# Kernel optimization log

Hardware: AMD Instinct MI355X
Metric: run time of the kernel (lower is better)

The kernel has to match this reference:

```python
import jax, jax.numpy as jnp
import numpy as np

N = 128
INSTANCES = 64
EMBED_DIM = 256
HIDDEN = 1024
BATCH = 2048


def _kaiming(key, dims):
    # matches custom_kaiming: randn * sqrt(2 / dims[-2])
    return jax.random.normal(key, dims, dtype=jnp.float32) * np.sqrt(2.0 / float(dims[-2])).astype(np.float32)


def setup_inputs() -> dict:
    key = jax.random.key(0)
    k_a, k_el, k_er, k_lin, k_un = jax.random.split(key, 5)
    a = jax.random.randint(k_a, (BATCH, 2), 0, N, dtype=jnp.int64 if jax.config.jax_enable_x64 else jnp.int32)
    return {
        "a": a,
        "embedding_left": _kaiming(k_el, (INSTANCES, N, EMBED_DIM)),
        "embedding_right": _kaiming(k_er, (INSTANCES, N, EMBED_DIM)),
        "linear": _kaiming(k_lin, (INSTANCES, EMBED_DIM, HIDDEN)),
        "unembedding": _kaiming(k_un, (INSTANCES, HIDDEN, N)),
    }


def reference(a, embedding_left, embedding_right, linear, unembedding):
    # one-hot @ embedding == direct gather along the vocab axis (same math, O(1) per lookup)
    a1, a2 = a[:, 0], a[:, 1]
    # [instances, batch, embed] -> [batch, instances, embed]
    x1 = jnp.transpose(jnp.take(embedding_left, a1, axis=1), (1, 0, 2))
    x2 = jnp.transpose(jnp.take(embedding_right, a2, axis=1), (1, 0, 2))
    hidden = jnp.einsum('bie,ieh->bih', x1 + x2, linear)
    out = jnp.einsum('bih,ihn->bin', jax.nn.gelu(hidden, approximate=False), unembedding)
    return out
```

## Files before the change

### kernel.cpp

```cpp
#include <hip/hip_runtime.h>
#include <hip/hip_bf16.h>

typedef __bf16 bf16;
typedef __bf16 bf16x8 __attribute__((ext_vector_type(8)));
typedef float  f32x4  __attribute__((ext_vector_type(4)));

#define MFMA16(A,B,C) __builtin_amdgcn_mfma_f32_16x16x32_bf16((A),(B),(C),0,0,0)

constexpr int NI    = 64;
constexpr int NN    = 128;
constexpr int E     = 256;
constexpr int HID   = 1024;
constexpr int BATCH = 2048;
constexpr int BM    = 128;
constexpr int BH    = 64;
constexpr int W1P   = E  + 8;
constexpr int W2P   = BH + 8;
constexpr int HP    = BH + 8;

__global__ __launch_bounds__(256) void transpose_cvt(
    const float* __restrict__ in, bf16* __restrict__ out, int R, int C)
{
    __shared__ bf16 t[64][74];
    const int inst = blockIdx.z;
    const int r0 = blockIdx.y * 64, c0 = blockIdx.x * 64;
    const float* ip = in + ((size_t)inst * R + r0) * C + c0;
    #pragma unroll
    for (int it = 0; it < 4; ++it) {
        int idx = it * 256 + threadIdx.x;
        int r = idx >> 4, c4 = idx & 15;
        f32x4 v = *(const f32x4*)(ip + (size_t)r * C + c4 * 4);
        #pragma unroll
        for (int k = 0; k < 4; ++k) t[r][c4 * 4 + k] = (bf16)v[k];
    }
    __syncthreads();
    bf16* op = out + ((size_t)inst * C + c0) * R + r0;
    #pragma unroll
    for (int it = 0; it < 2; ++it) {
        int idx = it * 256 + threadIdx.x;
        int c = idx >> 3, r8 = idx & 7;
        bf16x8 tmp;
        #pragma unroll
        for (int k = 0; k < 8; ++k) tmp[k] = t[r8 * 8 + k][c];
        *(bf16x8*)(op + (size_t)c * R + r8 * 8) = tmp;
    }
}

__device__ __forceinline__ float fast_gelu(float x) {
    float p = 1.5957691216f * __builtin_fmaf(0.044715f * x * x, x, x);
    return x * __builtin_amdgcn_rcpf(1.0f + __expf(-p));
}

template <bool PRET>
__global__ __launch_bounds__(256, 2) void mlp3_fused(
    const int*   __restrict__ a,
    const float* __restrict__ embL,
    const float* __restrict__ embR,
    const void*  __restrict__ W1v,
    const void*  __restrict__ W2v,
    float* __restrict__ out)
{
    __shared__ __align__(16) bf16 sW1[BH][W1P];
    __shared__ __align__(16) bf16 sW2[NN][W2P];
    __shared__ __align__(16) bf16 sH [BM][HP];
    static_assert(sizeof(bf16) * (BH * W1P + NN * W2P + BM * HP) <= 80 * 1024, "2 blocks/CU");

    const int blk   = blockIdx.x;
    const int xcd   = blk & 7;
    const int j     = blk >> 3;
    const int inst  = xcd + 8 * (j >> 4);
    const int btile = j & 15;

    const int tid  = threadIdx.x;
    const int wave = tid >> 6;
    const int lane = tid & 63;
    const int m = lane & 15;
    const int q = lane >> 4;

    bf16x8 aF[2][8];
    #pragma unroll
    for (int rt = 0; rt < 2; ++rt) {
        const int r  = btile * BM + wave * 32 + rt * 16 + m;
        const int i1 = a[2 * r + 0];
        const int i2 = a[2 * r + 1];
        const float* pl = embL + ((size_t)inst * NN + i1) * E;
        const float* pr = embR + ((size_t)inst * NN + i2) * E;
        #pragma unroll
        for (int ks = 0; ks < 8; ++ks) {
            const int e0 = ks * 32 + q * 8;
            f32x4 l0 = *(const f32x4*)(pl + e0);
            f32x4 l1 = *(const f32x4*)(pl + e0 + 4);
            f32x4 r0 = *(const f32x4*)(pr + e0);
            f32x4 r1 = *(const f32x4*)(pr + e0 + 4);
            bf16x8 s;
            #pragma unroll
            for (int k = 0; k < 4; ++k) {
                s[k]     = (bf16)(l0[k] + r0[k]);
                s[k + 4] = (bf16)(l1[k] + r1[k]);
            }
            aF[rt][ks] = s;
        }
    }

    f32x4 O[2][8];
    #pragma unroll
    for (int rt = 0; rt < 2; ++rt)
        #pragma unroll
        for (int ct = 0; ct < 8; ++ct)
            O[rt][ct] = (f32x4){0.f, 0.f, 0.f, 0.f};

    #pragma unroll 1
    for (int c = 0; c < HID / BH; ++c) {
        __syncthreads();
        if (PRET) {
            const bf16* W1 = (const bf16*)W1v;
            const bf16* W2 = (const bf16*)W2v;
            #pragma unroll
            for (int it = 0; it < 8; ++it) {
                const int idx = it * 256 + tid;
                const int hl = idx >> 5, e16 = idx & 31;
                *(bf16x8*)&sW1[hl][e16 * 8] =
                    *(const bf16x8*)(W1 + ((size_t)inst * HID + c * BH + hl) * E + e16 * 8);
            }
            #pragma unroll
            for (int it = 0; it < 4; ++it) {
                const int idx = it * 256 + tid;
                const int n = idx >> 3, h8 = idx & 7;
                *(bf16x8*)&sW2[n][h8 * 8] =
                    *(const bf16x8*)(W2 + ((size_t)inst * NN + n) * HID + c * BH + h8 * 8);
            }
        } else {
            const float* W1 = (const float*)W1v;
            const float* W2 = (const float*)W2v;
            #pragma unroll
            for (int it = 0; it < 8; ++it) {
                const int idx = it * 256 + tid;
                const int e = idx >> 3, h8 = idx & 7;
                f32x4 v0 = *(const f32x4*)(W1 + ((size_t)inst * E + e) * HID + c * BH + h8 * 8);
                f32x4 v1 = *(const f32x4*)(W1 + ((size_t)inst * E + e) * HID + c * BH + h8 * 8 + 4);
                #pragma unroll
                for (int k = 0; k < 4; ++k) {
                    sW1[h8 * 8 + k][e]     = (bf16)v0[k];
                    sW1[h8 * 8 + k + 4][e] = (bf16)v1[k];
                }
            }
            #pragma unroll
            for (int it = 0; it < 4; ++it) {
                const int idx = it * 256 + tid;
                const int h = idx >> 4, n8 = idx & 15;
                f32x4 v0 = *(const f32x4*)(W2 + ((size_t)inst * HID + c * BH + h) * NN + n8 * 8);
                f32x4 v1 = *(const f32x4*)(W2 + ((size_t)inst * HID + c * BH + h) * NN + n8 * 8 + 4);
                #pragma unroll
                for (int k = 0; k < 4; ++k) {
                    sW2[n8 * 8 + k][h]     = (bf16)v0[k];
                    sW2[n8 * 8 + k + 4][h] = (bf16)v1[k];
                }
            }
        }
        __syncthreads();

        f32x4 S[2][4];
        #pragma unroll
        for (int rt = 0; rt < 2; ++rt)
            #pragma unroll
            for (int ct = 0; ct < 4; ++ct) S[rt][ct] = (f32x4){0.f, 0.f, 0.f, 0.f};
        #pragma unroll
        for (int ks = 0; ks < 8; ++ks) {
            #pragma unroll
            for (int ct = 0; ct < 4; ++ct) {
                bf16x8 b = *(const bf16x8*)&sW1[ct * 16 + m][ks * 32 + q * 8];
                S[0][ct] = MFMA16(aF[0][ks], b, S[0][ct]);
                S[1][ct] = MFMA16(aF[1][ks], b, S[1][ct]);
            }
        }

        #pragma unroll
        for (int rt = 0; rt < 2; ++rt)
            #pragma unroll
            for (int ct = 0; ct < 4; ++ct)
                #pragma unroll
                for (int rr = 0; rr < 4; ++rr)
                    sH[wave * 32 + rt * 16 + q * 4 + rr][ct * 16 + m] =
                        (bf16)fast_gelu(S[rt][ct][rr]);
        asm volatile("s_waitcnt lgkmcnt(0)" ::: "memory");

        #pragma unroll
        for (int k2 = 0; k2 < 2; ++k2) {
            bf16x8 h0 = *(const bf16x8*)&sH[wave * 32 +  0 + m][k2 * 32 + q * 8];
            bf16x8 h1 = *(const bf16x8*)&sH[wave * 32 + 16 + m][k2 * 32 + q * 8];
            #pragma unroll
            for (int ct = 0; ct < 8; ++ct) {
                bf16x8 b = *(const bf16x8*)&sW2[ct * 16 + m][k2 * 32 + q * 8];
                O[0][ct] = MFMA16(h0, b, O[0][ct]);
                O[1][ct] = MFMA16(h1, b, O[1][ct]);
            }
        }
    }

    #pragma unroll
    for (int rt = 0; rt < 2; ++rt)
        #pragma unroll
        for (int ct = 0; ct < 8; ++ct)
            #pragma unroll
            for (int rr = 0; rr < 4; ++rr) {
                const int b = btile * BM + wave * 32 + rt * 16 + q * 4 + rr;
                const int n = ct * 16 + m;
                out[((size_t)b * NI + inst) * NN + n] = O[rt][ct][rr];
            }
}

extern "C" void kernel_launch(void* const* d_in, const int* in_sizes, int n_in,
                              void* d_out, int out_size, void* d_ws, size_t ws_size,
                              hipStream_t stream)
{
    const int*   a    = (const int*)d_in[0];
    const float* embL = (const float*)d_in[1];
    const float* embR = (const float*)d_in[2];
    const float* lin  = (const float*)d_in[3];
    const float* une  = (const float*)d_in[4];
    float* out = (float*)d_out;

    const size_t w1t_elems = (size_t)NI * HID * E;
    const size_t w2t_elems = (size_t)NI * NN * HID;
    const size_t need = (w1t_elems + w2t_elems) * sizeof(bf16);

    const int nblocks = (BATCH / BM) * NI;

    if (ws_size >= need) {
        bf16* w1t = (bf16*)d_ws;
        bf16* w2t = w1t + w1t_elems;
        transpose_cvt<<<dim3(HID / 64, E / 64, NI), 256, 0, stream>>>(
            lin, w1t, E, HID);
        transpose_cvt<<<dim3(NN / 64, HID / 64, NI), 256, 0, stream>>>(
            une, w2t, HID, NN);
        mlp3_fused<true><<<nblocks, 256, 0, stream>>>(
            a, embL, embR, (const void*)w1t, (const void*)w2t, out);
    } else {
        mlp3_fused<false><<<nblocks, 256, 0, stream>>>(
            a, embL, embR, (const void*)lin, (const void*)une, out);
    }
}
```

Measured before the change: 314.1 us.

## Drop weight pre-transpose kernels; load fp32 weights and transpose in-register

Removes the two transpose_cvt launches that converted the weights to transposed bf16 in a workspace. The fused kernel now reads the fp32 weights directly and does a 4x4 register transpose, writing bf16x4 vectors into shared memory instead of scalar stores. This saves the extra kernel launches and the round trip through the workspace. In exchange the main kernel reads twice as many weight bytes, since each of the 16 batch-tile blocks per instance re-reads fp32 weights.

```diff
diff --git a/kernel.cpp b/kernel.cpp
--- a/kernel.cpp
+++ b/kernel.cpp
@@ -2,6 +2,7 @@
 #include <hip/hip_bf16.h>
 
 typedef __bf16 bf16;
+typedef __bf16 bf16x4 __attribute__((ext_vector_type(4)));
 typedef __bf16 bf16x8 __attribute__((ext_vector_type(8)));
 typedef float  f32x4  __attribute__((ext_vector_type(4)));
 
@@ -18,52 +19,22 @@
 constexpr int W2P   = BH + 8;
 constexpr int HP    = BH + 8;
 
-__global__ __launch_bounds__(256) void transpose_cvt(
-    const float* __restrict__ in, bf16* __restrict__ out, int R, int C)
-{
-    __shared__ bf16 t[64][74];
-    const int inst = blockIdx.z;
-    const int r0 = blockIdx.y * 64, c0 = blockIdx.x * 64;
-    const float* ip = in + ((size_t)inst * R + r0) * C + c0;
-    #pragma unroll
-    for (int it = 0; it < 4; ++it) {
-        int idx = it * 256 + threadIdx.x;
-        int r = idx >> 4, c4 = idx & 15;
-        f32x4 v = *(const f32x4*)(ip + (size_t)r * C + c4 * 4);
-        #pragma unroll
-        for (int k = 0; k < 4; ++k) t[r][c4 * 4 + k] = (bf16)v[k];
-    }
-    __syncthreads();
-    bf16* op = out + ((size_t)inst * C + c0) * R + r0;
-    #pragma unroll
-    for (int it = 0; it < 2; ++it) {
-        int idx = it * 256 + threadIdx.x;
-        int c = idx >> 3, r8 = idx & 7;
-        bf16x8 tmp;
-        #pragma unroll
-        for (int k = 0; k < 8; ++k) tmp[k] = t[r8 * 8 + k][c];
-        *(bf16x8*)(op + (size_t)c * R + r8 * 8) = tmp;
-    }
-}
-
 __device__ __forceinline__ float fast_gelu(float x) {
     float p = 1.5957691216f * __builtin_fmaf(0.044715f * x * x, x, x);
     return x * __builtin_amdgcn_rcpf(1.0f + __expf(-p));
 }
 
-template <bool PRET>
 __global__ __launch_bounds__(256, 2) void mlp3_fused(
     const int*   __restrict__ a,
     const float* __restrict__ embL,
     const float* __restrict__ embR,
-    const void*  __restrict__ W1v,
-    const void*  __restrict__ W2v,
+    const float* __restrict__ W1,
+    const float* __restrict__ W2,
     float* __restrict__ out)
 {
     __shared__ __align__(16) bf16 sW1[BH][W1P];
     __shared__ __align__(16) bf16 sW2[NN][W2P];
     __shared__ __align__(16) bf16 sH [BM][HP];
-    static_assert(sizeof(bf16) * (BH * W1P + NN * W2P + BM * HP) <= 80 * 1024, "2 blocks/CU");
 
     const int blk   = blockIdx.x;
     const int xcd   = blk & 7;
@@ -109,51 +80,46 @@
         for (int ct = 0; ct < 8; ++ct)
             O[rt][ct] = (f32x4){0.f, 0.f, 0.f, 0.f};
 
+    const int w1_h0 = (tid & 15) * 4;
+    const int w1_eq = (tid >> 4) * 4;
+    const int w2_n0 = (tid & 31) * 4;
+    const int w2_hq = (tid >> 5) * 4;
+
     #pragma unroll 1
     for (int c = 0; c < HID / BH; ++c) {
         __syncthreads();
-        if (PRET) {
-            const bf16* W1 = (const bf16*)W1v;
-            const bf16* W2 = (const bf16*)W2v;
+
+        {
+            const float* base = W1 + ((size_t)inst * E + w1_eq) * HID + c * BH + w1_h0;
             #pragma unroll
-            for (int it = 0; it < 8; ++it) {
-                const int idx = it * 256 + tid;
-                const int hl = idx >> 5, e16 = idx & 31;
-                *(bf16x8*)&sW1[hl][e16 * 8] =
-                    *(const bf16x8*)(W1 + ((size_t)inst * HID + c * BH + hl) * E + e16 * 8);
-            }
-            #pragma unroll
-            for (int it = 0; it < 4; ++it) {
-                const int idx = it * 256 + tid;
-                const int n = idx >> 3, h8 = idx & 7;
-                *(bf16x8*)&sW2[n][h8 * 8] =
-                    *(const bf16x8*)(W2 + ((size_t)inst * NN + n) * HID + c * BH + h8 * 8);
-            }
-        } else {
-            const float* W1 = (const float*)W1v;
-            const float* W2 = (const float*)W2v;
-            #pragma unroll
-            for (int it = 0; it < 8; ++it) {
-                const int idx = it * 256 + tid;
-                const int e = idx >> 3, h8 = idx & 7;
-                f32x4 v0 = *(const f32x4*)(W1 + ((size_t)inst * E + e) * HID + c * BH + h8 * 8);
-                f32x4 v1 = *(const f32x4*)(W1 + ((size_t)inst * E + e) * HID + c * BH + h8 * 8 + 4);
+            for (int s = 0; s < 4; ++s) {
+                f32x4 v[4];
                 #pragma unroll
-                for (int k = 0; k < 4; ++k) {
-                    sW1[h8 * 8 + k][e]     = (bf16)v0[k];
-                    sW1[h8 * 8 + k + 4][e] = (bf16)v1[k];
+                for (int k = 0; k < 4; ++k)
+                    v[k] = *(const f32x4*)(base + ((size_t)s * 64 + k) * HID);
+                #pragma unroll
+                for (int jj = 0; jj < 4; ++jj) {
+                    bf16x4 w;
+                    #pragma unroll
+                    for (int k = 0; k < 4; ++k) w[k] = (bf16)v[k][jj];
+                    *(bf16x4*)&sW1[w1_h0 + jj][s * 64 + w1_eq] = w;
                 }
             }
+        }
+        {
+            const float* base = W2 + ((size_t)inst * HID + c * BH + w2_hq) * NN + w2_n0;
             #pragma unroll
-            for (int it = 0; it < 4; ++it) {
-                const int idx = it * 256 + tid;
-                const int h = idx >> 4, n8 = idx & 15;
-                f32x4 v0 = *(const f32x4*)(W2 + ((size_t)inst * HID + c * BH + h) * NN + n8 * 8);
-                f32x4 v1 = *(const f32x4*)(W2 + ((size_t)inst * HID + c * BH + h) * NN + n8 * 8 + 4);
+            for (int s = 0; s < 2; ++s) {
+                f32x4 v[4];
                 #pragma unroll
-                for (int k = 0; k < 4; ++k) {
-                    sW2[n8 * 8 + k][h]     = (bf16)v0[k];
-                    sW2[n8 * 8 + k + 4][h] = (bf16)v1[k];
+                for (int k = 0; k < 4; ++k)
+                    v[k] = *(const f32x4*)(base + ((size_t)s * 32 + k) * NN);
+                #pragma unroll
+                for (int jj = 0; jj < 4; ++jj) {
+                    bf16x4 w;
+                    #pragma unroll
+                    for (int k = 0; k < 4; ++k) w[k] = (bf16)v[k][jj];
+                    *(bf16x4*)&sW2[w2_n0 + jj][s * 32 + w2_hq] = w;
                 }
             }
         }
@@ -220,23 +186,6 @@
     const float* une  = (const float*)d_in[4];
     float* out = (float*)d_out;
 
-    const size_t w1t_elems = (size_t)NI * HID * E;
-    const size_t w2t_elems = (size_t)NI * NN * HID;
-    const size_t need = (w1t_elems + w2t_elems) * sizeof(bf16);
-
     const int nblocks = (BATCH / BM) * NI;
-
-    if (ws_size >= need) {
-        bf16* w1t = (bf16*)d_ws;
-        bf16* w2t = w1t + w1t_elems;
-        transpose_cvt<<<dim3(HID / 64, E / 64, NI), 256, 0, stream>>>(
-            lin, w1t, E, HID);
-        transpose_cvt<<<dim3(NN / 64, HID / 64, NI), 256, 0, stream>>>(
-            une, w2t, HID, NN);
-        mlp3_fused<true><<<nblocks, 256, 0, stream>>>(
-            a, embL, embR, (const void*)w1t, (const void*)w2t, out);
-    } else {
-        mlp3_fused<false><<<nblocks, 256, 0, stream>>>(
-            a, embL, embR, (const void*)lin, (const void*)une, out);
-    }
+    mlp3_fused<<<nblocks, 256, 0, stream>>>(a, embL, embR, lin, une, out);
 }
```

Result: slower. 353.5 us (+12.5%).
